# Kernel optimization log

Measured on AMD Instinct MI355X. Metric: run time of the kernel, lower is better.

Reference implementation:

```python
import jax, jax.numpy as jnp
import numpy as np

GRID_RANGE = ((-3.0, 3.0), (-3.0, 3.0))
GRID_SHAPE = (64, 64)
INIT_LENGTHSCALE = 0.1


def _construct_grid():
    axes = [jnp.linspace(lo, hi, s, dtype=jnp.float32)
            for (lo, hi), s in zip(GRID_RANGE, GRID_SHAPE)]
    mesh = jnp.meshgrid(*axes, indexing='ij')
    return jnp.stack(mesh, axis=-1)  # [64, 64, dx]


def setup_inputs() -> dict:
    key = jax.random.key(0)
    k1, k2 = jax.random.split(key)
    m, n, dx, dz = 8, 4096, 2, 16
    x = jax.random.normal(k1, (m, n, dx), dtype=jnp.float32)
    z = jax.random.normal(k2, (m, n, dz), dtype=jnp.float32)
    # lengthscale_param = log(exp(init_lengthscale) - 1), per dim
    ls_param = jnp.log(jnp.expm1(jnp.full((dx,), INIT_LENGTHSCALE, dtype=jnp.float32)))
    grid = _construct_grid()
    return {"x": x, "z": z, "lengthscale_param": ls_param, "grid": grid}


def reference(x, z, lengthscale_param, grid):
    # lengthscale = 1e-5 + softplus(param), per input dim
    ls = 1e-5 + jax.nn.softplus(lengthscale_param)  # [dx]
    m = x.shape[0]
    grid_flat = grid.reshape(-1, grid.shape[-1])  # [M, dx]
    # per-dim scaled differences; sum((g-x)^2 / ls^2) == sum(((g-x)/ls)^2)
    diff = (grid_flat[None, :, None, :] - x[:, None, :, :]) / ls  # [m, M, n, dx]
    pre_exp = jnp.sum(diff * diff, axis=-1)                        # [m, M, n]
    weights = jnp.exp(-0.5 * pre_exp)                              # [m, M, n]
    z_grid_flat = jnp.einsum('bmn,bnd->bmd', weights, z)           # [m, M, dz]
    z_grid = z_grid_flat.reshape((m,) + grid.shape[:-1] + (z.shape[-1],))
    x_grid = jnp.broadcast_to(grid[None], (m,) + grid.shape)
    return (x_grid, z_grid)
```

## Files before the change

### kernel.cpp

```cpp
#include <hip/hip_runtime.h>
#include <hip/hip_bf16.h>
#include <cstdint>

#define N_PTS   4096
#define M_GRID  4096
#define SKIP_E0 -20.0f

typedef __attribute__((ext_vector_type(8))) short  short8;
typedef __attribute__((ext_vector_type(4))) float  floatx4;

#define SMEM_BYTES 32772

__device__ __forceinline__ float bits_hi_f(uint32_t u) {
    union { uint32_t u; float f; } c; c.u = u & 0xffff0000u; return c.f;
}
__device__ __forceinline__ float bits_f(uint32_t u) {
    union { uint32_t u; float f; } c; c.u = u; return c.f;
}
__device__ __forceinline__ uint32_t pack_bf2(float a, float b) {
    union { __hip_bfloat162 h; uint32_t u; } c;
    c.h = __float22bfloat162_rn(make_float2(a, b));
    return c.u;
}

__global__ __launch_bounds__(512, 4)
void setconv_kernel(const float2* __restrict__ x2,
                    const float*  __restrict__ zf,
                    const float*  __restrict__ lsp,
                    const float2* __restrict__ grid2,
                    float2*       __restrict__ outx,
                    float*        __restrict__ outz)
{
    __shared__ __align__(16) char smem[SMEM_BYTES];
    uint2*   rec  = reinterpret_cast<uint2*>(smem);
    floatx4* redv = reinterpret_cast<floatx4*>(smem);
    int*     cntp = reinterpret_cast<int*>(smem + 32768);

    const int tid  = threadIdx.x;
    const int lane = tid & 63;
    const int w    = tid >> 6;
    const int mt   = w & 3;
    const int ks   = w >> 2;
    const int q    = lane >> 4;
    const int dn   = lane & 15;
    const int gtile = blockIdx.x;
    const int b     = blockIdx.y;

    float p0 = lsp[0], p1 = lsp[1];
    float sp0 = (p0 > 0.f) ? (p0 + log1pf(expf(-p0))) : log1pf(expf(p0));
    float sp1 = (p1 > 0.f) ? (p1 + log1pf(expf(-p1))) : log1pf(expf(p1));
    float ls0 = 1e-5f + sp0, ls1 = 1e-5f + sp1;
    const float q0 = -0.5f / (ls0 * ls0);
    const float q1 = -0.5f / (ls1 * ls1);

    const float2 gv = grid2[gtile * 64 + lane];
    const float  g0 = gv.x;
    if (w == 0) outx[(size_t)b * M_GRID + gtile * 64 + lane] = gv;
    const float g1m = grid2[gtile * 64 + mt * 16 + dn].y;

    if (tid == 0) *cntp = 0;
    __syncthreads();

    const float2* xb = x2 + b * N_PTS;

    for (int t = tid; t < N_PTS; t += 512) {
        float2 xv = xb[t];
        float d0 = g0 - xv.x;
        float e0 = q0 * d0 * d0;
        bool keep = (e0 >= SKIP_E0);
        unsigned long long m = __ballot(keep);
        int base = 0;
        if (lane == 0 && m) base = atomicAdd(cntp, __popcll(m));
        base = __shfl(base, 0);
        if (keep) {
            int off = __popcll(m & ((1ull << lane) - 1ull));
            __hip_bfloat16 hx = __float2bfloat16(xv.y);
            uint32_t x1n = ((uint32_t)*reinterpret_cast<uint16_t*>(&hx) << 16)
                         | (uint32_t)t;
            union { float f; uint32_t u; } ee; ee.f = e0;
            rec[base + off] = make_uint2(ee.u, x1n);
        }
    }
    __syncthreads();
    const int C    = *cntp;
    const int Cpad = (C + 63) & ~63;
    for (int t = C + tid; t < Cpad; t += 512) {
        union { float f; uint32_t u; } ee; ee.f = -1e30f;
        rec[t] = make_uint2(ee.u, 0u);
    }
    __syncthreads();

    const int ngroup = Cpad >> 6;
    const float* zcol = zf + (size_t)b * (N_PTS * 16) + dn;

    floatx4 acc = {0.f, 0.f, 0.f, 0.f};

    for (int gi = 0; gi < ngroup; ++gi) {
        const int k0 = (gi << 6) + (ks << 5) + (q << 3);
        const uint4* rq = reinterpret_cast<const uint4*>(rec + k0);
        uint4 r0 = rq[0], r1 = rq[1], r2 = rq[2], r3 = rq[3];

        float z0 = zcol[(size_t)(r0.y & 0xffffu) * 16];
        float z1 = zcol[(size_t)(r0.w & 0xffffu) * 16];
        float z2 = zcol[(size_t)(r1.y & 0xffffu) * 16];
        float z3 = zcol[(size_t)(r1.w & 0xffffu) * 16];
        float z4 = zcol[(size_t)(r2.y & 0xffffu) * 16];
        float z5 = zcol[(size_t)(r2.w & 0xffffu) * 16];
        float z6 = zcol[(size_t)(r3.y & 0xffffu) * 16];
        float z7 = zcol[(size_t)(r3.w & 0xffffu) * 16];

        float u0 = g1m - bits_hi_f(r0.y), u1 = g1m - bits_hi_f(r0.w);
        float u2 = g1m - bits_hi_f(r1.y), u3 = g1m - bits_hi_f(r1.w);
        float u4 = g1m - bits_hi_f(r2.y), u5 = g1m - bits_hi_f(r2.w);
        float u6 = g1m - bits_hi_f(r3.y), u7 = g1m - bits_hi_f(r3.w);
        float w0 = __expf(fmaf(q1 * u0, u0, bits_f(r0.x)));
        float w1 = __expf(fmaf(q1 * u1, u1, bits_f(r0.z)));
        float w2 = __expf(fmaf(q1 * u2, u2, bits_f(r1.x)));
        float w3 = __expf(fmaf(q1 * u3, u3, bits_f(r1.z)));
        float w4 = __expf(fmaf(q1 * u4, u4, bits_f(r2.x)));
        float w5 = __expf(fmaf(q1 * u5, u5, bits_f(r2.z)));
        float w6 = __expf(fmaf(q1 * u6, u6, bits_f(r3.x)));
        float w7 = __expf(fmaf(q1 * u7, u7, bits_f(r3.z)));

        union { uint32_t u[4]; short8 s; } af, bf;
        af.u[0] = pack_bf2(w0, w1); af.u[1] = pack_bf2(w2, w3);
        af.u[2] = pack_bf2(w4, w5); af.u[3] = pack_bf2(w6, w7);
        bf.u[0] = pack_bf2(z0, z1); bf.u[1] = pack_bf2(z2, z3);
        bf.u[2] = pack_bf2(z4, z5); bf.u[3] = pack_bf2(z6, z7);

        acc = __builtin_amdgcn_mfma_f32_16x16x32_bf16(af.s, bf.s, acc, 0, 0, 0);
    }

    __syncthreads();
    if (w >= 4) redv[(w - 4) * 64 + lane] = acc;
    __syncthreads();
    if (w < 4) {
        acc += redv[mt * 64 + lane];
        size_t base = ((size_t)b * M_GRID + gtile * 64 + mt * 16 + q * 4) * 16 + dn;
#pragma unroll
        for (int r = 0; r < 4; ++r)
            outz[base + (size_t)r * 16] = acc[r];
    }
}

extern "C" void kernel_launch(void* const* d_in, const int* in_sizes, int n_in,
                              void* d_out, int out_size, void* d_ws, size_t ws_size,
                              hipStream_t stream) {
    const float2* x2    = (const float2*)d_in[0];
    const float*  zf    = (const float*)d_in[1];
    const float*  lsp   = (const float*)d_in[2];
    const float2* grid2 = (const float2*)d_in[3];
    float* out = (float*)d_out;

    hipLaunchKernelGGL(setconv_kernel, dim3(64, 8), dim3(512), 0, stream,
                       x2, zf, lsp, grid2, (float2*)out, out + 65536);
}
```

Measured before the change: 90.00 us.

## Software-pipeline record and z gathers, use exp2 and split record layout

Prefetches the next group's shared-memory records and issues the z gathers for the following iteration after the MFMA, so global-load latency overlaps the exp/MFMA work. Stores records as float2 (e0, full-precision x1) plus a separate ushort array of pre-scaled indices, and folds log2(e) into the quadratic coefficients so exp2f can be used directly. Block-to-tile mapping is swizzled by batch to spread grid tiles. The cost is more shared memory and more live registers, which may affect occupancy.

```diff
diff --git a/kernel.cpp b/kernel.cpp
--- a/kernel.cpp
+++ b/kernel.cpp
@@ -4,19 +4,17 @@
 
 #define N_PTS   4096
 #define M_GRID  4096
-#define SKIP_E0 -20.0f
+#define LOG2E   1.4426950408889634f
+#define SKIP_E0L (-28.853900817779268f)
 
 typedef __attribute__((ext_vector_type(8))) short  short8;
 typedef __attribute__((ext_vector_type(4))) float  floatx4;
 
-#define SMEM_BYTES 32772
+#define OFF_EX   0
+#define OFF_NN   32768
+#define OFF_CNT  40960
+#define SMEM_BYTES 40964
 
-__device__ __forceinline__ float bits_hi_f(uint32_t u) {
-    union { uint32_t u; float f; } c; c.u = u & 0xffff0000u; return c.f;
-}
-__device__ __forceinline__ float bits_f(uint32_t u) {
-    union { uint32_t u; float f; } c; c.u = u; return c.f;
-}
 __device__ __forceinline__ uint32_t pack_bf2(float a, float b) {
     union { __hip_bfloat162 h; uint32_t u; } c;
     c.h = __float22bfloat162_rn(make_float2(a, b));
@@ -32,9 +30,10 @@
                     float*        __restrict__ outz)
 {
     __shared__ __align__(16) char smem[SMEM_BYTES];
-    uint2*   rec  = reinterpret_cast<uint2*>(smem);
+    float2*  ex   = reinterpret_cast<float2*>(smem + OFF_EX);
+    ushort*  nn   = reinterpret_cast<ushort*>(smem + OFF_NN);
+    int*     cntp = reinterpret_cast<int*>(smem + OFF_CNT);
     floatx4* redv = reinterpret_cast<floatx4*>(smem);
-    int*     cntp = reinterpret_cast<int*>(smem + 32768);
 
     const int tid  = threadIdx.x;
     const int lane = tid & 63;
@@ -43,15 +42,15 @@
     const int ks   = w >> 2;
     const int q    = lane >> 4;
     const int dn   = lane & 15;
-    const int gtile = blockIdx.x;
-    const int b     = blockIdx.y;
+    const int b    = blockIdx.y;
+    const int gtile = (int)((blockIdx.x + ((b & 4) ? 32u : 0u)) & 63u);
 
     float p0 = lsp[0], p1 = lsp[1];
     float sp0 = (p0 > 0.f) ? (p0 + log1pf(expf(-p0))) : log1pf(expf(p0));
     float sp1 = (p1 > 0.f) ? (p1 + log1pf(expf(-p1))) : log1pf(expf(p1));
     float ls0 = 1e-5f + sp0, ls1 = 1e-5f + sp1;
-    const float q0 = -0.5f / (ls0 * ls0);
-    const float q1 = -0.5f / (ls1 * ls1);
+    const float q0L = -0.5f * LOG2E / (ls0 * ls0);
+    const float q1L = -0.5f * LOG2E / (ls1 * ls1);
 
     const float2 gv = grid2[gtile * 64 + lane];
     const float  g0 = gv.x;
@@ -66,69 +65,90 @@
     for (int t = tid; t < N_PTS; t += 512) {
         float2 xv = xb[t];
         float d0 = g0 - xv.x;
-        float e0 = q0 * d0 * d0;
-        bool keep = (e0 >= SKIP_E0);
+        float e0 = q0L * d0 * d0;
+        bool keep = (e0 >= SKIP_E0L);
         unsigned long long m = __ballot(keep);
         int base = 0;
         if (lane == 0 && m) base = atomicAdd(cntp, __popcll(m));
         base = __shfl(base, 0);
         if (keep) {
-            int off = __popcll(m & ((1ull << lane) - 1ull));
-            __hip_bfloat16 hx = __float2bfloat16(xv.y);
-            uint32_t x1n = ((uint32_t)*reinterpret_cast<uint16_t*>(&hx) << 16)
-                         | (uint32_t)t;
-            union { float f; uint32_t u; } ee; ee.f = e0;
-            rec[base + off] = make_uint2(ee.u, x1n);
+            int off = base + __popcll(m & ((1ull << lane) - 1ull));
+            ex[off] = make_float2(e0, xv.y);
+            nn[off] = (ushort)(t << 4);
         }
     }
     __syncthreads();
     const int C    = *cntp;
     const int Cpad = (C + 63) & ~63;
     for (int t = C + tid; t < Cpad; t += 512) {
-        union { float f; uint32_t u; } ee; ee.f = -1e30f;
-        rec[t] = make_uint2(ee.u, 0u);
+        ex[t] = make_float2(-1e30f, 0.f);
+        nn[t] = 0;
     }
     __syncthreads();
 
     const int ngroup = Cpad >> 6;
-    const float* zcol = zf + (size_t)b * (N_PTS * 16) + dn;
+    const float* zb = zf + (size_t)b * (N_PTS * 16);
 
     floatx4 acc = {0.f, 0.f, 0.f, 0.f};
 
-    for (int gi = 0; gi < ngroup; ++gi) {
-        const int k0 = (gi << 6) + (ks << 5) + (q << 3);
-        const uint4* rq = reinterpret_cast<const uint4*>(rec + k0);
-        uint4 r0 = rq[0], r1 = rq[1], r2 = rq[2], r3 = rq[3];
+    if (ngroup > 0) {
+        const float4* e4 = reinterpret_cast<const float4*>(ex);
 
-        float z0 = zcol[(size_t)(r0.y & 0xffffu) * 16];
-        float z1 = zcol[(size_t)(r0.w & 0xffffu) * 16];
-        float z2 = zcol[(size_t)(r1.y & 0xffffu) * 16];
-        float z3 = zcol[(size_t)(r1.w & 0xffffu) * 16];
-        float z4 = zcol[(size_t)(r2.y & 0xffffu) * 16];
-        float z5 = zcol[(size_t)(r2.w & 0xffffu) * 16];
-        float z6 = zcol[(size_t)(r3.y & 0xffffu) * 16];
-        float z7 = zcol[(size_t)(r3.w & 0xffffu) * 16];
+        float4 A, B, Cc, D; uint4 N;
+        float a0, a1, a2, a3, a4, a5, a6, a7;
 
-        float u0 = g1m - bits_hi_f(r0.y), u1 = g1m - bits_hi_f(r0.w);
-        float u2 = g1m - bits_hi_f(r1.y), u3 = g1m - bits_hi_f(r1.w);
-        float u4 = g1m - bits_hi_f(r2.y), u5 = g1m - bits_hi_f(r2.w);
-        float u6 = g1m - bits_hi_f(r3.y), u7 = g1m - bits_hi_f(r3.w);
-        float w0 = __expf(fmaf(q1 * u0, u0, bits_f(r0.x)));
-        float w1 = __expf(fmaf(q1 * u1, u1, bits_f(r0.z)));
-        float w2 = __expf(fmaf(q1 * u2, u2, bits_f(r1.x)));
-        float w3 = __expf(fmaf(q1 * u3, u3, bits_f(r1.z)));
-        float w4 = __expf(fmaf(q1 * u4, u4, bits_f(r2.x)));
-        float w5 = __expf(fmaf(q1 * u5, u5, bits_f(r2.z)));
-        float w6 = __expf(fmaf(q1 * u6, u6, bits_f(r3.x)));
-        float w7 = __expf(fmaf(q1 * u7, u7, bits_f(r3.z)));
+#define LDREC(gi, A_, B_, C_, D_, N_) do {                                  \
+        int k0_ = ((gi) << 6) + (ks << 5) + (q << 3);                       \
+        int h_  = k0_ >> 1;                                                 \
+        A_ = e4[h_]; B_ = e4[h_ + 1]; C_ = e4[h_ + 2]; D_ = e4[h_ + 3];     \
+        N_ = *reinterpret_cast<const uint4*>(nn + k0_);                     \
+    } while (0)
 
-        union { uint32_t u[4]; short8 s; } af, bf;
-        af.u[0] = pack_bf2(w0, w1); af.u[1] = pack_bf2(w2, w3);
-        af.u[2] = pack_bf2(w4, w5); af.u[3] = pack_bf2(w6, w7);
-        bf.u[0] = pack_bf2(z0, z1); bf.u[1] = pack_bf2(z2, z3);
-        bf.u[2] = pack_bf2(z4, z5); bf.u[3] = pack_bf2(z6, z7);
+#define LDZ(N_) do {                                                        \
+        a0 = zb[(int)((N_).x & 0xffffu) + dn];                              \
+        a1 = zb[(int)((N_).x >> 16)     + dn];                              \
+        a2 = zb[(int)((N_).y & 0xffffu) + dn];                              \
+        a3 = zb[(int)((N_).y >> 16)     + dn];                              \
+        a4 = zb[(int)((N_).z & 0xffffu) + dn];                              \
+        a5 = zb[(int)((N_).z >> 16)     + dn];                              \
+        a6 = zb[(int)((N_).w & 0xffffu) + dn];                              \
+        a7 = zb[(int)((N_).w >> 16)     + dn];                              \
+    } while (0)
 
-        acc = __builtin_amdgcn_mfma_f32_16x16x32_bf16(af.s, bf.s, acc, 0, 0, 0);
+        LDREC(0, A, B, Cc, D, N);
+        LDZ(N);
+
+        for (int gi = 0; gi < ngroup; ++gi) {
+            const int nx = (gi + 1 < ngroup) ? gi + 1 : gi;
+            float4 A2, B2, C2, D2; uint4 N2;
+            LDREC(nx, A2, B2, C2, D2, N2);
+
+            float u0 = g1m - A.y,  u1 = g1m - A.w;
+            float u2 = g1m - B.y,  u3 = g1m - B.w;
+            float u4 = g1m - Cc.y, u5 = g1m - Cc.w;
+            float u6 = g1m - D.y,  u7 = g1m - D.w;
+            float w0 = exp2f(fmaf(q1L * u0, u0, A.x));
+            float w1 = exp2f(fmaf(q1L * u1, u1, A.z));
+            float w2 = exp2f(fmaf(q1L * u2, u2, B.x));
+            float w3 = exp2f(fmaf(q1L * u3, u3, B.z));
+            float w4 = exp2f(fmaf(q1L * u4, u4, Cc.x));
+            float w5 = exp2f(fmaf(q1L * u5, u5, Cc.z));
+            float w6 = exp2f(fmaf(q1L * u6, u6, D.x));
+            float w7 = exp2f(fmaf(q1L * u7, u7, D.z));
+
+            union { uint32_t u[4]; short8 s; } af, bf;
+            af.u[0] = pack_bf2(w0, w1); af.u[1] = pack_bf2(w2, w3);
+            af.u[2] = pack_bf2(w4, w5); af.u[3] = pack_bf2(w6, w7);
+            bf.u[0] = pack_bf2(a0, a1); bf.u[1] = pack_bf2(a2, a3);
+            bf.u[2] = pack_bf2(a4, a5); bf.u[3] = pack_bf2(a6, a7);
+
+            acc = __builtin_amdgcn_mfma_f32_16x16x32_bf16(af.s, bf.s, acc, 0, 0, 0);
+
+            LDZ(N2);
+            A = A2; B = B2; Cc = C2; D = D2;
+        }
+#undef LDREC
+#undef LDZ
     }
 
     __syncthreads();
```

After: 83.41 us. -7.3%, faster.
